# Kernel optimization log

Hardware: AMD Instinct MI355X
Metric: run time of the kernel (lower is better)

The kernel has to match this reference:

```python
import jax, jax.numpy as jnp
import numpy as np

B, L, D = 8192, 200, 64
NUM_ITEMS = 100000
HID = 64  # attention hidden_dim


def setup_inputs() -> dict:
    key = jax.random.key(0)
    ks = jax.random.split(key, 16)
    inp = {
        "item_sequence": jax.random.randint(ks[0], (B, L), 0, NUM_ITEMS),
        "click_sequence": jax.random.randint(ks[1], (B, L), 0, 2),
        "seq_length": jax.random.randint(ks[2], (B, 1), 1, L + 1),
        "target_item": jax.random.randint(ks[3], (B, 1), 0, NUM_ITEMS),
        "context_features": jax.random.normal(ks[4], (B, 9), dtype=jnp.float32),
        # embedding table (num_items+1, D)
        "emb_table": jax.random.normal(ks[5], (NUM_ITEMS + 1, D), dtype=jnp.float32) * 0.05,
        # attention MLP: Linear(2D->64), Linear(64->32), Linear(32->1)
        "aw1": jax.random.normal(ks[6], (2 * D, HID), dtype=jnp.float32) * 0.05,
        "ab1": jnp.zeros((HID,), jnp.float32),
        "aw2": jax.random.normal(ks[7], (HID, HID // 2), dtype=jnp.float32) * 0.05,
        "ab2": jnp.zeros((HID // 2,), jnp.float32),
        "aw3": jax.random.normal(ks[8], (HID // 2, 1), dtype=jnp.float32) * 0.05,
        "ab3": jnp.zeros((1,), jnp.float32),
        # context MLP: Linear(9->32)
        "cw": jax.random.normal(ks[9], (9, 32), dtype=jnp.float32) * 0.05,
        "cb": jnp.zeros((32,), jnp.float32),
        # head MLP: Linear(160->128), Linear(128->64), Linear(64->1)
        "mw1": jax.random.normal(ks[10], (2 * D + 32, 128), dtype=jnp.float32) * 0.05,
        "mb1": jnp.zeros((128,), jnp.float32),
        "mw2": jax.random.normal(ks[11], (128, 64), dtype=jnp.float32) * 0.05,
        "mb2": jnp.zeros((64,), jnp.float32),
        "mw3": jax.random.normal(ks[12], (64, 1), dtype=jnp.float32) * 0.05,
        "mb3": jnp.zeros((1,), jnp.float32),
    }
    return inp


def reference(item_sequence, click_sequence, seq_length, target_item, context_features,
              emb_table, aw1, ab1, aw2, ab2, aw3, ab3, cw, cb,
              mw1, mb1, mw2, mb2, mw3, mb3):
    seq_emb = emb_table[item_sequence]                 # [B, L, D]
    tgt_emb = emb_table[target_item[:, 0]]             # [B, D]
    seq_len = item_sequence.shape[1]
    mask = (jnp.arange(seq_len)[None, :] < seq_length).astype(seq_emb.dtype)  # [B, L]

    # DIN attention: concat(query, keys) -> 3-layer MLP -> masked softmax -> weighted sum
    q = jnp.broadcast_to(tgt_emb[:, None, :], seq_emb.shape)          # [B, L, D]
    att_in = jnp.concatenate([q, seq_emb], axis=-1)                   # [B, L, 2D]
    h = jax.nn.relu(att_in @ aw1 + ab1)
    h = jax.nn.relu(h @ aw2 + ab2)
    scores = (h @ aw3 + ab3)[..., 0]                                  # [B, L]
    scores = jnp.where(mask == 0, jnp.asarray(-1e9, scores.dtype), scores)
    w = jax.nn.softmax(scores, axis=1)                                # [B, L]
    attended = jnp.einsum('bl,bld->bd', w, seq_emb)                   # [B, D]

    ctx = jax.nn.relu(context_features @ cw + cb)                     # [B, 32]
    comb = jnp.concatenate([attended, tgt_emb, ctx], axis=1)          # [B, 2D+32]
    h = jax.nn.relu(comb @ mw1 + mb1)
    h = jax.nn.relu(h @ mw2 + mb2)
    out = jax.nn.sigmoid(h @ mw3 + mb3)[:, 0]                         # [B]
    return out
```

## Files before the change

kernel.cpp:

```cpp
#include <hip/hip_runtime.h>
#include <cmath>

typedef __attribute__((ext_vector_type(8))) short s16x8;
typedef __attribute__((ext_vector_type(4))) short s16x4;
typedef __attribute__((ext_vector_type(4))) float f32x4;

__device__ __forceinline__ short f2bf(float f) {
    union { float f; unsigned u; } v; v.f = f;
    unsigned r = v.u + 0x7FFFu + ((v.u >> 16) & 1u);
    return (short)(r >> 16);
}
__device__ __forceinline__ float bf2f(short s) {
    union { unsigned u; float f; } v; v.u = ((unsigned)(unsigned short)s) << 16;
    return v.f;
}
__device__ __forceinline__ unsigned cvtpk2(float lo, float hi) {
    unsigned r;
    asm("v_cvt_pk_bf16_f32 %0, %1, %2" : "=v"(r) : "v"(lo), "v"(hi));
    return r;
}
__device__ __forceinline__ s16x8 cvt8(float4 a, float4 b) {
    union { s16x8 v; unsigned u[4]; } r;
    r.u[0] = cvtpk2(a.x, a.y);
    r.u[1] = cvtpk2(a.z, a.w);
    r.u[2] = cvtpk2(b.x, b.y);
    r.u[3] = cvtpk2(b.z, b.w);
    return r.v;
}

#define W1SEQ_SH  0
#define W1TOP_SH  4096
#define W2_SH     8192
#define MW1T_SH   10240
#define MW2T_SH   30720
#define QC_F      19456
#define CB_SH     1087488

__global__ __launch_bounds__(256)
void din_wprep_kernel(const float* __restrict__ aw1,
                      const float* __restrict__ aw2,
                      const float* __restrict__ mw1,
                      const float* __restrict__ mw2,
                      short* __restrict__ ws)
{
    const int g  = blockIdx.x >> 3;
    const int sb = blockIdx.x & 7;
    const int t  = threadIdx.x;
    if (g == 0) {
        for (int idx = sb * 512 + t; idx < sb * 512 + 512; idx += 256) {
            int j = idx & 7, lane = (idx >> 3) & 63, fr = idx >> 9;
            int n = (fr >> 1) * 16 + (lane & 15);
            int k = (fr & 1) * 32 + (lane >> 4) * 8 + j;
            ws[W1SEQ_SH + idx] = f2bf(aw1[(64 + k) * 64 + n]);
        }
    } else if (g == 1) {
        for (int idx = sb * 512 + t; idx < sb * 512 + 512; idx += 256) {
            int j = idx & 7, lane = (idx >> 3) & 63, fr = idx >> 9;
            int n = (fr >> 1) * 16 + (lane & 15);
            int k = (fr & 1) * 32 + (lane >> 4) * 8 + j;
            ws[W1TOP_SH + idx] = f2bf(aw1[k * 64 + n]);
        }
    } else if (g == 2) {
        int idx = sb * 256 + t;
        int j = idx & 7, lane = (idx >> 3) & 63, fr = idx >> 9;
        int n = (fr >> 1) * 16 + (lane & 15);
        int k = (fr & 1) * 32 + (lane >> 4) * 8 + j;
        ws[W2_SH + idx] = f2bf(aw2[k * 32 + n]);
    } else if (g == 3) {
        for (int idx = sb * 1024 + t; idx < sb * 1024 + 1024; idx += 256) {
            int j = idx & 7, lane = (idx >> 3) & 63, fr = idx >> 9;
            int n = (fr >> 2) * 16 + (lane & 15);
            int k = (fr & 3) * 32 + (lane >> 4) * 8 + j;
            ws[MW2T_SH + idx] = f2bf(mw2[k * 64 + n]);
        }
    } else {
        const int base = ((g - 4) * 8 + sb) * 640;
        for (int ii = t; ii < 640; ii += 256) {
            int idx = base + ii;
            int j = idx & 7, lane = (idx >> 3) & 63, fr = idx >> 9;
            int nt = fr / 5, ks = fr - nt * 5;
            int n = nt * 16 + (lane & 15);
            int k = ks * 32 + (lane >> 4) * 8 + j;
            ws[MW1T_SH + idx] = f2bf(mw1[k * 128 + n]);
        }
    }
}

__global__ __launch_bounds__(256)
void din_qc_kernel(const int* __restrict__ tgt_item,
                   const float* __restrict__ emb,
                   const float* __restrict__ ab1,
                   short* __restrict__ ws)
{
    const int t = threadIdx.x, lane = t & 63, wave = t >> 6;
    const int quad = lane >> 4, r16 = lane & 15;
    const short* w1t = ws + W1TOP_SH;
    float* qc = (float*)ws + QC_F;

    const int b0 = (blockIdx.x * 4 + wave) * 16;
    const int it = tgt_item[b0 + r16];
    const float* rp = emb + it * 64 + quad * 8;
    float4 v0 = *(const float4*)(rp),      v1 = *(const float4*)(rp + 4);
    float4 v2 = *(const float4*)(rp + 32), v3 = *(const float4*)(rp + 36);
    s16x8 a0 = cvt8(v0, v1);
    s16x8 a1 = cvt8(v2, v3);

    f32x4 acc[4] = {{0,0,0,0},{0,0,0,0},{0,0,0,0},{0,0,0,0}};
    #pragma unroll
    for (int nt = 0; nt < 4; ++nt) {
        s16x8 b_0 = *(const s16x8*)(w1t + ((nt * 2 + 0) * 64 + lane) * 8);
        s16x8 b_1 = *(const s16x8*)(w1t + ((nt * 2 + 1) * 64 + lane) * 8);
        acc[nt] = __builtin_amdgcn_mfma_f32_16x16x32_bf16(a0, b_0, acc[nt], 0, 0, 0);
        acc[nt] = __builtin_amdgcn_mfma_f32_16x16x32_bf16(a1, b_1, acc[nt], 0, 0, 0);
    }
    #pragma unroll
    for (int nt = 0; nt < 4; ++nt) {
        float bias = ab1[nt * 16 + r16];
        #pragma unroll
        for (int rr = 0; rr < 4; ++rr)
            qc[(b0 + quad * 4 + rr) * 64 + nt * 16 + r16] = acc[nt][rr] + bias;
    }
}

#define H1_PITCH 72
__global__ __launch_bounds__(256)
void din_att_v3(const int* __restrict__ item_seq,
                const int* __restrict__ seq_len_p,
                const int* __restrict__ tgt_item,
                const float* __restrict__ ctx_feat,
                const float* __restrict__ emb,
                const float* __restrict__ ab2,
                const float* __restrict__ aw3, const float* __restrict__ ab3,
                const float* __restrict__ cw,  const float* __restrict__ cb,
                short* __restrict__ ws)
{
    const int t = threadIdx.x, lane = t & 63, wave = t >> 6;
    const int quad = lane >> 4, r16 = lane & 15;
    __shared__ short s_w1[4096];
    __shared__ short s_h1[4][16 * H1_PITCH];
    __shared__ float s_sc[4][64];
    __shared__ float s_pool[4][64];
    __shared__ float s_m[4], s_e[4];

    const int b   = blockIdx.x;
    const int len = seq_len_p[b];
    const int tgt = tgt_item[b];

    {
        const s16x8* src = (const s16x8*)(ws + W1SEQ_SH);
        s16x8* dst = (s16x8*)s_w1;
        dst[t]       = src[t];
        dst[t + 256] = src[t + 256];
    }

    bool act[4];
    s16x8 af[4][2];
    #pragma unroll
    for (int ci = 0; ci < 4; ++ci) {
        const int c = wave + ci * 4;
        act[ci] = (c < 13) && (c * 16 < len);
        if (act[ci]) {
            int r = c * 16 + r16; if (r > 199) r = 199;
            const int it = item_seq[b * 200 + r];
            const float* rp = emb + it * 64 + quad * 8;
            float4 v0 = *(const float4*)(rp),      v1 = *(const float4*)(rp + 4);
            float4 v2 = *(const float4*)(rp + 32), v3 = *(const float4*)(rp + 36);
            af[ci][0] = cvt8(v0, v1);
            af[ci][1] = cvt8(v2, v3);
        }
    }
    s16x8 w2r[4];
    #pragma unroll
    for (int fr = 0; fr < 4; ++fr)
        w2r[fr] = *(const s16x8*)(ws + W2_SH + (fr * 64 + lane) * 8);
    const float* qcp = (const float*)ws + QC_F + b * 64;
    float qcv[4];
    #pragma unroll
    for (int nt = 0; nt < 4; ++nt) qcv[nt] = qcp[nt * 16 + r16];
    const float bias2_lo = ab2[r16], bias2_hi = ab2[16 + r16];
    const float w3_lo    = aw3[r16], w3_hi    = aw3[16 + r16];
    const float b3       = ab3[0];
    __syncthreads();

    short* h1w = s_h1[wave];

    #pragma unroll
    for (int ci = 0; ci < 4; ++ci) {
        if (!act[ci]) continue;
        f32x4 acc[4] = {{0,0,0,0},{0,0,0,0},{0,0,0,0},{0,0,0,0}};
        #pragma unroll
        for (int nt = 0; nt < 4; ++nt) {
            s16x8 b_0 = *(const s16x8*)&s_w1[((nt * 2 + 0) * 64 + lane) * 8];
            s16x8 b_1 = *(const s16x8*)&s_w1[((nt * 2 + 1) * 64 + lane) * 8];
            acc[nt] = __builtin_amdgcn_mfma_f32_16x16x32_bf16(af[ci][0], b_0, acc[nt], 0, 0, 0);
            acc[nt] = __builtin_amdgcn_mfma_f32_16x16x32_bf16(af[ci][1], b_1, acc[nt], 0, 0, 0);
        }
        #pragma unroll
        for (int nt = 0; nt < 4; ++nt) {
            float v0 = fmaxf(acc[nt][0] + qcv[nt], 0.f);
            float v1 = fmaxf(acc[nt][1] + qcv[nt], 0.f);
            float v2 = fmaxf(acc[nt][2] + qcv[nt], 0.f);
            float v3 = fmaxf(acc[nt][3] + qcv[nt], 0.f);
            unsigned p01 = cvtpk2(v0, v1), p23 = cvtpk2(v2, v3);
            const int col = nt * 16 + r16;
            h1w[(quad * 4 + 0) * H1_PITCH + col] = (short)p01;
            h1w[(quad * 4 + 1) * H1_PITCH + col] = (short)(p01 >> 16);
            h1w[(quad * 4 + 2) * H1_PITCH + col] = (short)p23;
            h1w[(quad * 4 + 3) * H1_PITCH + col] = (short)(p23 >> 16);
        }
        __builtin_amdgcn_wave_barrier();

        s16x8 h0  = *(const s16x8*)&h1w[r16 * H1_PITCH + quad * 8];
        s16x8 h1v = *(const s16x8*)&h1w[r16 * H1_PITCH + 32 + quad * 8];
        f32x4 c2[2] = {{0,0,0,0},{0,0,0,0}};
        #pragma unroll
        for (int nt = 0; nt < 2; ++nt) {
            c2[nt] = __builtin_amdgcn_mfma_f32_16x16x32_bf16(h0,  w2r[nt * 2],     c2[nt], 0, 0, 0);
            c2[nt] = __builtin_amdgcn_mfma_f32_16x16x32_bf16(h1v, w2r[nt * 2 + 1], c2[nt], 0, 0, 0);
        }
        #pragma unroll
        for (int rr = 0; rr < 4; ++rr) {
            float p = fmaxf(c2[0][rr] + bias2_lo, 0.f) * w3_lo
                    + fmaxf(c2[1][rr] + bias2_hi, 0.f) * w3_hi;
            p += __shfl_xor(p, 8);
            p += __shfl_xor(p, 4);
            p += __shfl_xor(p, 2);
            p += __shfl_xor(p, 1);
            if (r16 == 0) s_sc[wave][ci * 16 + quad * 4 + rr] = p + b3;
        }
        __builtin_amdgcn_wave_barrier();
    }

    const int ci_l = lane >> 4;
    const int c_l  = wave + ci_l * 4;
    const int grow = c_l * 16 + r16;
    const bool valid = (c_l < 13) && (grow < len);
    float sc = valid ? s_sc[wave][lane] : -1e30f;
    float m = sc;
    #pragma unroll
    for (int off = 32; off; off >>= 1) m = fmaxf(m, __shfl_xor(m, off));
    float e = valid ? __expf(sc - m) : 0.f;
    #pragma unroll
    for (int off = 32; off; off >>= 1) e += __shfl_xor(e, off);

    float p[16];
    #pragma unroll
    for (int i = 0; i < 16; ++i) p[i] = 0.f;
    #pragma unroll
    for (int ci = 0; ci < 4; ++ci) {
        if (!act[ci]) continue;
        const int row = (wave + ci * 4) * 16 + r16;
        const float w = (row < len) ? __expf(s_sc[wave][ci * 16 + r16] - m) : 0.f;
        #pragma unroll
        for (int j = 0; j < 8; ++j) {
            p[j]     += w * bf2f(af[ci][0][j]);
            p[8 + j] += w * bf2f(af[ci][1][j]);
        }
    }
    #pragma unroll
    for (int i = 0; i < 16; ++i) {
        p[i] += __shfl_xor(p[i], 1);
        p[i] += __shfl_xor(p[i], 2);
        p[i] += __shfl_xor(p[i], 4);
        p[i] += __shfl_xor(p[i], 8);
    }
    if (r16 == 0) {
        #pragma unroll
        for (int j = 0; j < 8; ++j) {
            s_pool[wave][quad * 8 + j]      = p[j];
            s_pool[wave][32 + quad * 8 + j] = p[8 + j];
        }
    }
    if (lane == 0) { s_m[wave] = m; s_e[wave] = e; }
    __syncthreads();

    short* comb = ws + CB_SH + b * 160;
    if (t < 64) {
        float gm = fmaxf(fmaxf(s_m[0], s_m[1]), fmaxf(s_m[2], s_m[3]));
        float s0 = __expf(s_m[0] - gm), s1 = __expf(s_m[1] - gm);
        float s2 = __expf(s_m[2] - gm), s3 = __expf(s_m[3] - gm);
        float denom = s0 * s_e[0] + s1 * s_e[1] + s2 * s_e[2] + s3 * s_e[3];
        float pooled = s0 * s_pool[0][t] + s1 * s_pool[1][t]
                     + s2 * s_pool[2][t] + s3 * s_pool[3][t];
        comb[t] = f2bf(pooled / denom);
    } else if (t < 96) {
        const int j = t - 64;
        float a = cb[j];
        #pragma unroll
        for (int k = 0; k < 9; ++k) a += ctx_feat[b * 9 + k] * cw[k * 32 + j];
        comb[128 + j] = f2bf(fmaxf(a, 0.f));
    } else if (t < 160) {
        comb[64 + (t - 96)] = f2bf(emb[tgt * 64 + (t - 96)]);
    }
}

__global__ __launch_bounds__(256)
void din_mlp_kernel(const float* __restrict__ mb1,
                    const float* __restrict__ mb2,
                    const float* __restrict__ mw3, const float* __restrict__ mb3,
                    const short* __restrict__ ws,
                    float* __restrict__ out)
{
    const int t = threadIdx.x, lane = t & 63, wave = t >> 6;
    const int quad = lane >> 4, r16 = lane & 15;
    __shared__ short s_h1[16 * 136];
    __shared__ short s_h2[16 * 72];

    const int b0 = blockIdx.x * 16;
    const short* comb = ws + CB_SH;
    const short* w1   = ws + MW1T_SH;
    const short* w2   = ws + MW2T_SH;

    s16x8 a[5];
    #pragma unroll
    for (int ks = 0; ks < 5; ++ks)
        a[ks] = *(const s16x8*)(comb + (b0 + r16) * 160 + ks * 32 + quad * 8);
    f32x4 acc[2] = {{0,0,0,0},{0,0,0,0}};
    #pragma unroll
    for (int ntl = 0; ntl < 2; ++ntl) {
        const int nt = wave * 2 + ntl;
        #pragma unroll
        for (int ks = 0; ks < 5; ++ks) {
            s16x8 bf = *(const s16x8*)(w1 + ((nt * 5 + ks) * 64 + lane) * 8);
            acc[ntl] = __builtin_amdgcn_mfma_f32_16x16x32_bf16(a[ks], bf, acc[ntl], 0, 0, 0);
        }
    }
    #pragma unroll
    for (int ntl = 0; ntl < 2; ++ntl) {
        const int nt = wave * 2 + ntl;
        float bias = mb1[nt * 16 + r16];
        float v0 = fmaxf(acc[ntl][0] + bias, 0.f);
        float v1 = fmaxf(acc[ntl][1] + bias, 0.f);
        float v2 = fmaxf(acc[ntl][2] + bias, 0.f);
        float v3 = fmaxf(acc[ntl][3] + bias, 0.f);
        unsigned p01 = cvtpk2(v0, v1), p23 = cvtpk2(v2, v3);
        const int col = nt * 16 + r16;
        s_h1[(quad * 4 + 0) * 136 + col] = (short)p01;
        s_h1[(quad * 4 + 1) * 136 + col] = (short)(p01 >> 16);
        s_h1[(quad * 4 + 2) * 136 + col] = (short)p23;
        s_h1[(quad * 4 + 3) * 136 + col] = (short)(p23 >> 16);
    }
    __syncthreads();

    s16x8 a2[4];
    #pragma unroll
    for (int ks = 0; ks < 4; ++ks)
        a2[ks] = *(const s16x8*)&s_h1[r16 * 136 + ks * 32 + quad * 8];
    f32x4 acc2 = {0,0,0,0};
    {
        const int nt = wave;
        #pragma unroll
        for (int ks = 0; ks < 4; ++ks) {
            s16x8 bf = *(const s16x8*)(w2 + ((nt * 4 + ks) * 64 + lane) * 8);
            acc2 = __builtin_amdgcn_mfma_f32_16x16x32_bf16(a2[ks], bf, acc2, 0, 0, 0);
        }
        float bias = mb2[nt * 16 + r16];
        float v0 = fmaxf(acc2[0] + bias, 0.f);
        float v1 = fmaxf(acc2[1] + bias, 0.f);
        float v2 = fmaxf(acc2[2] + bias, 0.f);
        float v3 = fmaxf(acc2[3] + bias, 0.f);
        unsigned p01 = cvtpk2(v0, v1), p23 = cvtpk2(v2, v3);
        const int col = nt * 16 + r16;
        s_h2[(quad * 4 + 0) * 72 + col] = (short)p01;
        s_h2[(quad * 4 + 1) * 72 + col] = (short)(p01 >> 16);
        s_h2[(quad * 4 + 2) * 72 + col] = (short)p23;
        s_h2[(quad * 4 + 3) * 72 + col] = (short)(p23 >> 16);
    }
    __syncthreads();

    if (wave == 0) {
        float p = 0.f;
        #pragma unroll
        for (int j = 0; j < 16; ++j)
            p += bf2f(s_h2[r16 * 72 + quad * 16 + j]) * mw3[quad * 16 + j];
        p += __shfl_xor(p, 16);
        p += __shfl_xor(p, 32);
        if (quad == 0) out[b0 + r16] = 1.f / (1.f + __expf(-(p + mb3[0])));
    }
}

extern "C" void kernel_launch(void* const* d_in, const int* in_sizes, int n_in,
                              void* d_out, int out_size, void* d_ws, size_t ws_size,
                              hipStream_t stream)
{
    const int*   item_seq  = (const int*)  d_in[0];
    const int*   seq_len   = (const int*)  d_in[2];
    const int*   tgt_item  = (const int*)  d_in[3];
    const float* ctx_feat  = (const float*)d_in[4];
    const float* emb       = (const float*)d_in[5];
    const float* aw1 = (const float*)d_in[6];
    const float* ab1 = (const float*)d_in[7];
    const float* aw2 = (const float*)d_in[8];
    const float* ab2 = (const float*)d_in[9];
    const float* aw3 = (const float*)d_in[10];
    const float* ab3 = (const float*)d_in[11];
    const float* cw  = (const float*)d_in[12];
    const float* cb  = (const float*)d_in[13];
    const float* mw1 = (const float*)d_in[14];
    const float* mb1 = (const float*)d_in[15];
    const float* mw2 = (const float*)d_in[16];
    const float* mb2 = (const float*)d_in[17];
    const float* mw3 = (const float*)d_in[18];
    const float* mb3 = (const float*)d_in[19];
    float* out = (float*)d_out;
    short* ws  = (short*)d_ws;

    hipLaunchKernelGGL(din_wprep_kernel, dim3(64), dim3(256), 0, stream,
                       aw1, aw2, mw1, mw2, ws);
    hipLaunchKernelGGL(din_qc_kernel, dim3(128), dim3(256), 0, stream,
                       tgt_item, emb, ab1, ws);
    hipLaunchKernelGGL(din_att_v3, dim3(8192), dim3(256), 0, stream,
                       item_seq, seq_len, tgt_item, ctx_feat, emb,
                       ab2, aw3, ab3, cw, cb, ws);
    hipLaunchKernelGGL(din_mlp_kernel, dim3(512), dim3(256), 0, stream,
                       mb1, mb2, mw3, mb3, ws, out);
}
```

Measured before the change: 188.8 us.

## Pre-convert embedding table to bf16 in workspace before gathers

Adds a pass in the weight-prep kernel that converts the whole fp32 embedding table (100001x64) into a bf16 copy in workspace. The attention and query kernels then gather bf16 rows directly, which halves the bytes per random gather and drops the per-row conversion. In exchange, every call reads 25.6MB and writes 12.8MB to convert the full table. The old fp32 path is kept as a fallback when the workspace is too small.

```diff
diff --git a/kernel.cpp b/kernel.cpp
--- a/kernel.cpp
+++ b/kernel.cpp
@@ -35,17 +35,31 @@
 #define MW2T_SH   30720
 #define QC_F      19456
 #define CB_SH     1087488
+#define EMB_SH    2400256
+#define EMB_ROWS  100001
+#define EMB_VEC8  800008
 
 __global__ __launch_bounds__(256)
 void din_wprep_kernel(const float* __restrict__ aw1,
                       const float* __restrict__ aw2,
                       const float* __restrict__ mw1,
                       const float* __restrict__ mw2,
+                      const float* __restrict__ emb,
                       short* __restrict__ ws)
 {
+    const int t = threadIdx.x;
+    if (blockIdx.x >= 64) {
+        const int idx = (blockIdx.x - 64) * 256 + t;
+        if (idx < EMB_VEC8) {
+            const float* rp = emb + (size_t)idx * 8;
+            float4 v0 = *(const float4*)(rp);
+            float4 v1 = *(const float4*)(rp + 4);
+            *(s16x8*)(ws + EMB_SH + (size_t)idx * 8) = cvt8(v0, v1);
+        }
+        return;
+    }
     const int g  = blockIdx.x >> 3;
     const int sb = blockIdx.x & 7;
-    const int t  = threadIdx.x;
     if (g == 0) {
         for (int idx = sb * 512 + t; idx < sb * 512 + 512; idx += 256) {
             int j = idx & 7, lane = (idx >> 3) & 63, fr = idx >> 9;
@@ -86,6 +100,7 @@
     }
 }
 
+template<bool TAB>
 __global__ __launch_bounds__(256)
 void din_qc_kernel(const int* __restrict__ tgt_item,
                    const float* __restrict__ emb,
@@ -99,11 +114,18 @@
 
     const int b0 = (blockIdx.x * 4 + wave) * 16;
     const int it = tgt_item[b0 + r16];
-    const float* rp = emb + it * 64 + quad * 8;
-    float4 v0 = *(const float4*)(rp),      v1 = *(const float4*)(rp + 4);
-    float4 v2 = *(const float4*)(rp + 32), v3 = *(const float4*)(rp + 36);
-    s16x8 a0 = cvt8(v0, v1);
-    s16x8 a1 = cvt8(v2, v3);
+    s16x8 a0, a1;
+    if constexpr (TAB) {
+        const short* rp = ws + EMB_SH + (size_t)it * 64 + quad * 8;
+        a0 = *(const s16x8*)(rp);
+        a1 = *(const s16x8*)(rp + 32);
+    } else {
+        const float* rp = emb + (size_t)it * 64 + quad * 8;
+        float4 v0 = *(const float4*)(rp),      v1 = *(const float4*)(rp + 4);
+        float4 v2 = *(const float4*)(rp + 32), v3 = *(const float4*)(rp + 36);
+        a0 = cvt8(v0, v1);
+        a1 = cvt8(v2, v3);
+    }
 
     f32x4 acc[4] = {{0,0,0,0},{0,0,0,0},{0,0,0,0},{0,0,0,0}};
     #pragma unroll
@@ -123,6 +145,7 @@
 }
 
 #define H1_PITCH 72
+template<bool TAB>
 __global__ __launch_bounds__(256)
 void din_att_v3(const int* __restrict__ item_seq,
                 const int* __restrict__ seq_len_p,
@@ -162,11 +185,17 @@
         if (act[ci]) {
             int r = c * 16 + r16; if (r > 199) r = 199;
             const int it = item_seq[b * 200 + r];
-            const float* rp = emb + it * 64 + quad * 8;
-            float4 v0 = *(const float4*)(rp),      v1 = *(const float4*)(rp + 4);
-            float4 v2 = *(const float4*)(rp + 32), v3 = *(const float4*)(rp + 36);
-            af[ci][0] = cvt8(v0, v1);
-            af[ci][1] = cvt8(v2, v3);
+            if constexpr (TAB) {
+                const short* rp = ws + EMB_SH + (size_t)it * 64 + quad * 8;
+                af[ci][0] = *(const s16x8*)(rp);
+                af[ci][1] = *(const s16x8*)(rp + 32);
+            } else {
+                const float* rp = emb + (size_t)it * 64 + quad * 8;
+                float4 v0 = *(const float4*)(rp),      v1 = *(const float4*)(rp + 4);
+                float4 v2 = *(const float4*)(rp + 32), v3 = *(const float4*)(rp + 36);
+                af[ci][0] = cvt8(v0, v1);
+                af[ci][1] = cvt8(v2, v3);
+            }
         }
     }
     s16x8 w2r[4];
@@ -290,7 +319,11 @@
         for (int k = 0; k < 9; ++k) a += ctx_feat[b * 9 + k] * cw[k * 32 + j];
         comb[128 + j] = f2bf(fmaxf(a, 0.f));
     } else if (t < 160) {
-        comb[64 + (t - 96)] = f2bf(emb[tgt * 64 + (t - 96)]);
+        if constexpr (TAB) {
+            comb[64 + (t - 96)] = ws[EMB_SH + (size_t)tgt * 64 + (t - 96)];
+        } else {
+            comb[64 + (t - 96)] = f2bf(emb[(size_t)tgt * 64 + (t - 96)]);
+        }
     }
 }
 
@@ -405,13 +438,26 @@
     float* out = (float*)d_out;
     short* ws  = (short*)d_ws;
 
-    hipLaunchKernelGGL(din_wprep_kernel, dim3(64), dim3(256), 0, stream,
-                       aw1, aw2, mw1, mw2, ws);
-    hipLaunchKernelGGL(din_qc_kernel, dim3(128), dim3(256), 0, stream,
-                       tgt_item, emb, ab1, ws);
-    hipLaunchKernelGGL(din_att_v3, dim3(8192), dim3(256), 0, stream,
-                       item_seq, seq_len, tgt_item, ctx_feat, emb,
-                       ab2, aw3, ab3, cw, cb, ws);
+    const size_t need_bytes = (size_t)(EMB_SH + EMB_ROWS * 64) * sizeof(short);
+    const bool tab = ws_size >= need_bytes;
+
+    if (tab) {
+        hipLaunchKernelGGL(din_wprep_kernel, dim3(64 + 3126), dim3(256), 0, stream,
+                           aw1, aw2, mw1, mw2, emb, ws);
+        hipLaunchKernelGGL(din_qc_kernel<true>, dim3(128), dim3(256), 0, stream,
+                           tgt_item, emb, ab1, ws);
+        hipLaunchKernelGGL(din_att_v3<true>, dim3(8192), dim3(256), 0, stream,
+                           item_seq, seq_len, tgt_item, ctx_feat, emb,
+                           ab2, aw3, ab3, cw, cb, ws);
+    } else {
+        hipLaunchKernelGGL(din_wprep_kernel, dim3(64), dim3(256), 0, stream,
+                           aw1, aw2, mw1, mw2, emb, ws);
+        hipLaunchKernelGGL(din_qc_kernel<false>, dim3(128), dim3(256), 0, stream,
+                           tgt_item, emb, ab1, ws);
+        hipLaunchKernelGGL(din_att_v3<false>, dim3(8192), dim3(256), 0, stream,
+                           item_seq, seq_len, tgt_item, ctx_feat, emb,
+                           ab2, aw3, ab3, cw, cb, ws);
+    }
     hipLaunchKernelGGL(din_mlp_kernel, dim3(512), dim3(256), 0, stream,
                        mb1, mb2, mw3, mb3, ws, out);
 }
```

Result: faster. 184.8 us (-2.1%).
